# Optimization experiments

Measured on AMD Instinct MI355X. Metric: run time of the kernel, lower is better.

Reference implementation:

```python
import jax, jax.numpy as jnp
import numpy as np

N_NODES = 100000
N_EDGES = 625000
D_IN = 128
D_OUT = 128
N_ETYPES = 64


def setup_inputs() -> dict:
    key = jax.random.key(0)
    k1, k2, k3, k4, k5, k6 = jax.random.split(key, 6)
    node_features = jax.random.normal(k1, (N_NODES, D_IN), dtype=jnp.float32)
    edge_index = jax.random.randint(k2, (2, N_EDGES), 0, N_NODES, dtype=jnp.int64)
    edge_type = jax.random.randint(k3, (N_EDGES,), 0, N_ETYPES, dtype=jnp.int64)
    edge_emb = jax.random.normal(k4, (N_ETYPES, D_OUT), dtype=jnp.float32)
    W = jax.random.normal(k5, (D_IN, D_OUT), dtype=jnp.float32) / np.sqrt(D_IN)
    b = jax.random.normal(k6, (D_OUT,), dtype=jnp.float32) * 0.01
    return {"node_features": node_features, "edge_index": edge_index,
            "edge_type": edge_type, "edge_emb": edge_emb, "W": W, "b": b}


def reference(node_features, edge_index, edge_type, edge_emb, W, b):
    # Linear transform of node features: (N, D_out)
    h = node_features @ W + b
    src, tgt = edge_index[0], edge_index[1]
    # Per-edge message: gather src feature + edge-type embedding  (E, D_out)
    messages = h[src] + edge_emb[edge_type]
    # Scatter-add into target nodes
    aggregated = jax.ops.segment_sum(messages, tgt, num_segments=N_NODES)
    # Self contribution + ReLU
    return jax.nn.relu(aggregated + h)
```

## Files before the change

kernel.cpp:

```cpp
#include <hip/hip_runtime.h>
#include <hip/hip_bf16.h>

#define D 128

typedef __attribute__((ext_vector_type(8))) short short8v;
typedef __attribute__((ext_vector_type(4))) float float4v;

__device__ __forceinline__ unsigned short f2bf(float f) {
  union { float f; unsigned int u; } v; v.f = f;
  unsigned int r = v.u + 0x7fffu + ((v.u >> 16) & 1u);
  return (unsigned short)(r >> 16);
}
__device__ __forceinline__ unsigned int pkbf(float lo, float hi) {
  float2 f; f.x = lo; f.y = hi;
  __hip_bfloat162 v = __float22bfloat162_rn(f);
  union { __hip_bfloat162 b; unsigned int u; } c; c.b = v;
  return c.u;
}
__device__ __forceinline__ float bflo(unsigned int u) {
  union { unsigned int v; float f; } c; c.v = u << 16; return c.f;
}
__device__ __forceinline__ float bfhi(unsigned int u) {
  union { unsigned int v; float f; } c; c.v = u & 0xffff0000u; return c.f;
}

__global__ __launch_bounds__(256) void prep_kernel(
    const float* __restrict__ W, const float* __restrict__ eemb,
    unsigned short* __restrict__ Wt, unsigned short* __restrict__ em_bf,
    unsigned short* __restrict__ h_bf, int* __restrict__ counts,
    int n_nodes) {
  int i = blockIdx.x * 256 + threadIdx.x;
  if (i < D * D) Wt[i] = f2bf(W[(i & 127) * D + (i >> 7)]);
  if (i < 64 * D) em_bf[i] = f2bf(eemb[i]);
  if (i < 64) ((unsigned int*)(h_bf + (size_t)n_nodes * D))[i] = 0u;
  if (i >= 64 && i < 128) ((unsigned int*)(em_bf + 64 * D))[i - 64] = 0u;
  if (i < n_nodes) counts[i] = 0;
}

#define XS_STRIDE 138
__global__ __launch_bounds__(256) void gemm_h_kernel(
    const float* __restrict__ nf, const unsigned short* __restrict__ Wt,
    const float* __restrict__ b, unsigned short* __restrict__ h_bf,
    const int* __restrict__ eidx_tgt, int* __restrict__ counts,
    int n_nodes, int n_edges, int epb) {
  __shared__ unsigned short Xs[64 * XS_STRIDE];
  const int tid = threadIdx.x;
  const int nodeBase = blockIdx.x * 64;

  #pragma unroll
  for (int s = 0; s < 4; ++s) {
    const int row = (tid >> 4) + s * 16;
    const int col = (tid & 15) * 8;
    uint4 sv = {0u, 0u, 0u, 0u};
    if (nodeBase + row < n_nodes) {
      const float4* p = (const float4*)&nf[(size_t)(nodeBase + row) * D + col];
      float4 a = p[0], c = p[1];
      sv.x = pkbf(a.x, a.y);
      sv.y = pkbf(a.z, a.w);
      sv.z = pkbf(c.x, c.y);
      sv.w = pkbf(c.z, c.w);
    }
    *(uint4*)&Xs[row * XS_STRIDE + col] = sv;
  }

  const int w = tid >> 6;
  const int l = tid & 63;
  const int m = l & 15;
  const int q = l >> 4;
  const int n0 = (w & 1) * 64;
  const int nodeHalf = (w >> 1) * 32;

  short8v afrag[4][4];
  #pragma unroll
  for (int nt = 0; nt < 4; ++nt) {
    const int n = n0 + nt * 16 + m;
    #pragma unroll
    for (int kc = 0; kc < 4; ++kc)
      afrag[nt][kc] = *(const short8v*)&Wt[n * D + kc * 32 + q * 8];
  }

  float4v acc[4][2] = {};
  __syncthreads();

  #pragma unroll
  for (int kc = 0; kc < 4; ++kc) {
    #pragma unroll
    for (int t = 0; t < 2; ++t) {
      const int node = nodeHalf + t * 16 + m;
      const short8v bv =
          *(const short8v*)&Xs[node * XS_STRIDE + kc * 32 + q * 8];
      #pragma unroll
      for (int nt = 0; nt < 4; ++nt)
        acc[nt][t] = __builtin_amdgcn_mfma_f32_16x16x32_bf16(
            afrag[nt][kc], bv, acc[nt][t], 0, 0, 0);
    }
  }

  #pragma unroll
  for (int nt = 0; nt < 4; ++nt) {
    const int colBase = n0 + nt * 16 + q * 4;
    const float4 bv = *(const float4*)&b[colBase];
    #pragma unroll
    for (int t = 0; t < 2; ++t) {
      const int node = nodeBase + nodeHalf + t * 16 + m;
      if (node < n_nodes) {
        uint2 val;
        val.x = pkbf(acc[nt][t][0] + bv.x, acc[nt][t][1] + bv.y);
        val.y = pkbf(acc[nt][t][2] + bv.z, acc[nt][t][3] + bv.w);
        *(uint2*)&h_bf[(size_t)node * D + colBase] = val;
      }
    }
  }

  const int ebase = blockIdx.x * epb;
  int eend = ebase + epb;
  if (eend > n_edges) eend = n_edges;
  for (int e = ebase + tid; e < eend; e += 256)
    atomicAdd(&counts[eidx_tgt[e]], 1);
}

__global__ __launch_bounds__(256) void scan1_kernel(
    const int* __restrict__ counts, int* __restrict__ offsets,
    int* __restrict__ blockSums, int n) {
  __shared__ int lds[256];
  const int tid = threadIdx.x;
  const int base = blockIdx.x * 1024 + tid * 4;
  int v[4];
  #pragma unroll
  for (int k = 0; k < 4; ++k) v[k] = (base + k < n) ? counts[base + k] : 0;
  int s = v[0] + v[1] + v[2] + v[3];
  lds[tid] = s;
  for (int off = 1; off < 256; off <<= 1) {
    __syncthreads();
    int t = (tid >= off) ? lds[tid - off] : 0;
    __syncthreads();
    lds[tid] += t;
  }
  __syncthreads();
  int run = lds[tid] - s;
  #pragma unroll
  for (int k = 0; k < 4; ++k) {
    if (base + k < n) offsets[base + k] = run;
    run += v[k];
  }
  if (tid == 255) blockSums[blockIdx.x] = lds[255];
}

__global__ __launch_bounds__(256) void scan23_kernel(
    int* __restrict__ offsets, int* __restrict__ cursor,
    const int* __restrict__ blockSums, int nb, int n, int n_edges) {
  __shared__ int lds[256];
  const int tid = threadIdx.x;
  const int bid = blockIdx.x;
  lds[tid] = (tid < bid && tid < nb) ? blockSums[tid] : 0;
  __syncthreads();
  #pragma unroll
  for (int off = 128; off > 0; off >>= 1) {
    if (tid < off) lds[tid] += lds[tid + off];
    __syncthreads();
  }
  const int add = lds[0];
  const int base = bid * 1024 + tid * 4;
  #pragma unroll
  for (int k = 0; k < 4; ++k) {
    int i = base + k;
    if (i < n) {
      int o = offsets[i] + add;
      offsets[i] = o;
      cursor[i] = o;
    }
  }
  if (bid == 0 && tid == 0) offsets[n] = n_edges;
}

__global__ __launch_bounds__(256) void scatter_kernel(
    const int* __restrict__ eidx, const int* __restrict__ etype,
    int* __restrict__ cursor, unsigned int* __restrict__ packed, int n_edges) {
  const int e0 = (blockIdx.x * 256 + threadIdx.x) * 4;
  if (e0 + 3 < n_edges) {
    const int4 s4 = *(const int4*)&eidx[e0];
    const int4 t4 = *(const int4*)&eidx[n_edges + e0];
    const int4 y4 = *(const int4*)&etype[e0];
    int pos;
    pos = atomicAdd(&cursor[t4.x], 1);
    packed[pos] = (unsigned int)s4.x | ((unsigned int)y4.x << 17);
    pos = atomicAdd(&cursor[t4.y], 1);
    packed[pos] = (unsigned int)s4.y | ((unsigned int)y4.y << 17);
    pos = atomicAdd(&cursor[t4.z], 1);
    packed[pos] = (unsigned int)s4.z | ((unsigned int)y4.z << 17);
    pos = atomicAdd(&cursor[t4.w], 1);
    packed[pos] = (unsigned int)s4.w | ((unsigned int)y4.w << 17);
  } else {
    for (int e = e0; e < n_edges; ++e) {
      const int pos = atomicAdd(&cursor[eidx[n_edges + e]], 1);
      packed[pos] = (unsigned int)eidx[e] | ((unsigned int)etype[e] << 17);
    }
  }
}

__global__ __launch_bounds__(256) void aggregate_kernel(
    const int* __restrict__ offsets, const unsigned int* __restrict__ packed,
    const uint2* __restrict__ e4, const uint2* __restrict__ h4,
    float* __restrict__ out, int n_nodes, int n_edges, unsigned int zero_p) {
  const int gid = blockIdx.x * 256 + threadIdx.x;
  const int lane = threadIdx.x & 63;
  const int half = lane >> 5;
  const int sl = lane & 31;
  const int n = (gid >> 6) * 2 + half;
  if (n >= n_nodes) return;

  const uint2 sb = h4[(size_t)n * 32 + sl];
  float a0 = bflo(sb.x), a1 = bfhi(sb.x), a2 = bflo(sb.y), a3 = bfhi(sb.y);
  float c0 = 0.f, c1 = 0.f, c2 = 0.f, c3 = 0.f;

  int j = offsets[n];
  const int end = offsets[n + 1];
  int trips = (end - j + 7) >> 3;
  int to = __shfl_xor(trips, 32);
  const int T = trips > to ? trips : to;
  const int emax = n_edges - 1;

  for (int t = 0; t < T; ++t, j += 8) {
    unsigned int p[8];
    #pragma unroll
    for (int u = 0; u < 8; ++u) {
      const int ju = j + u;
      const unsigned int pu = packed[ju <= emax ? ju : emax];
      p[u] = (ju < end) ? pu : zero_p;
    }
    uint2 g[8], ev[8];
    #pragma unroll
    for (int u = 0; u < 8; ++u)
      g[u] = h4[(size_t)(p[u] & 0x1FFFFu) * 32 + sl];
    #pragma unroll
    for (int u = 0; u < 8; ++u)
      ev[u] = e4[(p[u] >> 17) * 32 + sl];
    #pragma unroll
    for (int u = 0; u < 8; u += 2) {
      a0 += bflo(g[u].x) + bflo(ev[u].x);
      a1 += bfhi(g[u].x) + bfhi(ev[u].x);
      a2 += bflo(g[u].y) + bflo(ev[u].y);
      a3 += bfhi(g[u].y) + bfhi(ev[u].y);
      c0 += bflo(g[u + 1].x) + bflo(ev[u + 1].x);
      c1 += bfhi(g[u + 1].x) + bfhi(ev[u + 1].x);
      c2 += bflo(g[u + 1].y) + bflo(ev[u + 1].y);
      c3 += bfhi(g[u + 1].y) + bfhi(ev[u + 1].y);
    }
  }

  float4 r;
  r.x = fmaxf(a0 + c0, 0.f);
  r.y = fmaxf(a1 + c1, 0.f);
  r.z = fmaxf(a2 + c2, 0.f);
  r.w = fmaxf(a3 + c3, 0.f);
  ((float4*)out)[(size_t)n * 32 + sl] = r;
}

extern "C" void kernel_launch(void* const* d_in, const int* in_sizes, int n_in,
                              void* d_out, int out_size, void* d_ws,
                              size_t ws_size, hipStream_t stream) {
  const float* nf   = (const float*)d_in[0];
  const int*   eidx = (const int*)d_in[1];
  const int*   etyp = (const int*)d_in[2];
  const float* eemb = (const float*)d_in[3];
  const float* W    = (const float*)d_in[4];
  const float* b    = (const float*)d_in[5];

  const int n_nodes = in_sizes[0] / D;
  const int n_edges = in_sizes[2];

  float* out = (float*)d_out;

  char* base = (char*)d_ws;
  unsigned short* Wt = (unsigned short*)base;
  unsigned short* em_bf = (unsigned short*)(base + 32768);
  unsigned short* h_bf = (unsigned short*)(base + 65536);
  char* tail = base + 65536 + (size_t)(n_nodes + 1) * D * 2;
  int* counts = (int*)tail;
  int* offsets = counts + n_nodes;
  int* cursor = offsets + (n_nodes + 1);
  int* blockSums = cursor + n_nodes;
  unsigned int* packed = (unsigned int*)(blockSums + 1024);

  const int nb = (n_nodes + 1023) / 1024;
  const int gemmBlocks = (n_nodes + 63) / 64;
  const int epb = (n_edges + gemmBlocks - 1) / gemmBlocks;

  prep_kernel<<<(n_nodes + 255) / 256, 256, 0, stream>>>(W, eemb, Wt, em_bf,
                                                         h_bf, counts, n_nodes);

  gemm_h_kernel<<<gemmBlocks, 256, 0, stream>>>(
      nf, Wt, b, h_bf, eidx + n_edges, counts, n_nodes, n_edges, epb);

  scan1_kernel<<<nb, 256, 0, stream>>>(counts, offsets, blockSums, n_nodes);
  scan23_kernel<<<nb, 256, 0, stream>>>(offsets, cursor, blockSums, nb,
                                        n_nodes, n_edges);

  scatter_kernel<<<(n_edges + 1023) / 1024, 256, 0, stream>>>(
      eidx, etyp, cursor, packed, n_edges);

  const unsigned int zero_p = (unsigned int)n_nodes | (64u << 17);
  const int aggBlocks = (n_nodes + 7) / 8;
  aggregate_kernel<<<aggBlocks, 256, 0, stream>>>(
      offsets, packed, (const uint2*)em_bf, (const uint2*)h_bf, out, n_nodes,
      n_edges, zero_p);
}
```

Baseline: 143.3 us.

## Stage node features into LDS via async global_load_lds and overlap edge counting

The GEMM kernel now copies the fp32 node-feature tile straight into LDS with global_load_lds, using an XOR swizzle to avoid bank conflicts. Conversion to bf16 moves to the point where the MFMA operands are read. The per-edge target-count atomics now run before the MFMA phase, so they overlap with the asynchronous tile load instead of trailing the kernel. In exchange, the LDS footprint roughly doubles, since the tile is kept as fp32, which may lower occupancy. The bf16 conversion work is also repeated by both column-half waves.

```diff
diff --git a/kernel.cpp b/kernel.cpp
--- a/kernel.cpp
+++ b/kernel.cpp
@@ -37,38 +37,55 @@
   if (i < n_nodes) counts[i] = 0;
 }
 
-#define XS_STRIDE 138
 __global__ __launch_bounds__(256) void gemm_h_kernel(
     const float* __restrict__ nf, const unsigned short* __restrict__ Wt,
     const float* __restrict__ b, unsigned short* __restrict__ h_bf,
     const int* __restrict__ eidx_tgt, int* __restrict__ counts,
     int n_nodes, int n_edges, int epb) {
-  __shared__ unsigned short Xs[64 * XS_STRIDE];
+  __shared__ float Xs[64 * D];
   const int tid = threadIdx.x;
+  const int wv = tid >> 6;
+  const int ln = tid & 63;
   const int nodeBase = blockIdx.x * 64;
 
-  #pragma unroll
-  for (int s = 0; s < 4; ++s) {
-    const int row = (tid >> 4) + s * 16;
-    const int col = (tid & 15) * 8;
-    uint4 sv = {0u, 0u, 0u, 0u};
-    if (nodeBase + row < n_nodes) {
-      const float4* p = (const float4*)&nf[(size_t)(nodeBase + row) * D + col];
-      float4 a = p[0], c = p[1];
-      sv.x = pkbf(a.x, a.y);
-      sv.y = pkbf(a.z, a.w);
-      sv.z = pkbf(c.x, c.y);
-      sv.w = pkbf(c.z, c.w);
-    }
-    *(uint4*)&Xs[row * XS_STRIDE + col] = sv;
-  }
-
-  const int w = tid >> 6;
-  const int l = tid & 63;
-  const int m = l & 15;
-  const int q = l >> 4;
-  const int n0 = (w & 1) * 64;
-  const int nodeHalf = (w >> 1) * 32;
+  const char* nf_tile = (const char*)(nf + (size_t)nodeBase * D);
+  char* xs_b = (char*)Xs;
+
+  if (nodeBase + 64 <= n_nodes) {
+    #pragma unroll
+    for (int it = 0; it < 8; ++it) {
+      const int doff = wv * 8192 + it * 1024;
+      const int off = doff + ln * 16;
+      const int src = off ^ (((off >> 9) & 7) << 4);
+      __builtin_amdgcn_global_load_lds(
+          (const __attribute__((address_space(1))) unsigned int*)(nf_tile + src),
+          (__attribute__((address_space(3))) unsigned int*)(xs_b + doff),
+          16, 0, 0);
+    }
+  } else {
+    #pragma unroll
+    for (int it = 0; it < 8; ++it) {
+      const int off = (it * 256 + tid) * 16;
+      const int src = off ^ (((off >> 9) & 7) << 4);
+      const int row = src >> 9;
+      float4 v = {0.f, 0.f, 0.f, 0.f};
+      if (nodeBase + row < n_nodes) v = *(const float4*)(nf_tile + src);
+      *(float4*)(xs_b + off) = v;
+    }
+  }
+
+  {
+    const int ebase = blockIdx.x * epb;
+    int eend = ebase + epb;
+    if (eend > n_edges) eend = n_edges;
+    for (int e = ebase + tid; e < eend; e += 256)
+      atomicAdd(&counts[eidx_tgt[e]], 1);
+  }
+
+  const int m = ln & 15;
+  const int q = ln >> 4;
+  const int n0 = (wv & 1) * 64;
+  const int nodeHalf = (wv >> 1) * 32;
 
   short8v afrag[4][4];
   #pragma unroll
@@ -87,8 +104,16 @@
     #pragma unroll
     for (int t = 0; t < 2; ++t) {
       const int node = nodeHalf + t * 16 + m;
-      const short8v bv =
-          *(const short8v*)&Xs[node * XS_STRIDE + kc * 32 + q * 8];
+      const int ba = node * 512 + kc * 128 + q * 32;
+      const int sw = (node & 7) << 4;
+      const float4 x0 = *(const float4*)(xs_b + (ba ^ sw));
+      const float4 x1 = *(const float4*)(xs_b + ((ba + 16) ^ sw));
+      union { unsigned int u[4]; short8v s; } cv;
+      cv.u[0] = pkbf(x0.x, x0.y);
+      cv.u[1] = pkbf(x0.z, x0.w);
+      cv.u[2] = pkbf(x1.x, x1.y);
+      cv.u[3] = pkbf(x1.z, x1.w);
+      const short8v bv = cv.s;
       #pragma unroll
       for (int nt = 0; nt < 4; ++nt)
         acc[nt][t] = __builtin_amdgcn_mfma_f32_16x16x32_bf16(
@@ -111,12 +136,6 @@
       }
     }
   }
-
-  const int ebase = blockIdx.x * epb;
-  int eend = ebase + epb;
-  if (eend > n_edges) eend = n_edges;
-  for (int e = ebase + tid; e < eend; e += 256)
-    atomicAdd(&counts[eidx_tgt[e]], 1);
 }
 
 __global__ __launch_bounds__(256) void scan1_kernel(
```

After: 131.0 us. 1.09x faster.
